# Performance work log

Measured on AMD Instinct MI355X. Metric: run time of the kernel, lower is better.

The kernel has to match this reference:

```python
import jax, jax.numpy as jnp
import numpy as np

L, B, H, IN = 4, 256, 1024, 1024

def setup_inputs() -> dict:
    key = jax.random.key(0)
    ks = jax.random.split(key, 7)
    return {
        "x": jax.random.normal(ks[0], (B, IN), jnp.float32),
        "h0": jax.random.normal(ks[1], (L, B, H), jnp.float32),
        "c0": jax.random.normal(ks[2], (L, B, H), jnp.float32),
        "w_ih": jax.random.normal(ks[3], (L, 4 * H, IN), jnp.float32) * 0.02,
        "w_hh": jax.random.normal(ks[4], (L, 4 * H, H), jnp.float32) * 0.02,
        "b_ih": jax.random.normal(ks[5], (L, 4 * H), jnp.float32) * 0.02,
        "b_hh": jax.random.normal(ks[6], (L, 4 * H), jnp.float32) * 0.02,
    }

def _lstm_cell(inp, h, c, wi, wh, bi, bh):
    # gates: (B, 4H), PyTorch gate order i, f, g, o
    gates = jnp.dot(inp, wi.T) + jnp.dot(h, wh.T) + bi + bh
    i_g, f_g, g_g, o_g = jnp.split(gates, 4, axis=-1)
    c_new = jax.nn.sigmoid(f_g) * c + jax.nn.sigmoid(i_g) * jnp.tanh(g_g)
    h_new = jax.nn.sigmoid(o_g) * jnp.tanh(c_new)
    return h_new, c_new

def reference(x, h0, c0, w_ih, w_hh, b_ih, b_hh):
    # Sequential over layers (inter-layer dependency); dropout is identity (eval mode / p=0).
    inp = x
    hs, cs = [], []
    for i in range(h0.shape[0]):
        h, c = _lstm_cell(inp, h0[i], c0[i], w_ih[i], w_hh[i], b_ih[i], b_hh[i])
        hs.append(h)
        cs.append(c)
        inp = h
    return jnp.stack(hs, axis=0), jnp.stack(cs, axis=0)
```

## Files before the change

### kernel.cpp

```cpp
#include <hip/hip_runtime.h>

#define NLAYER 4
#define BATCH  256
#define HID    1024

typedef float f32x4 __attribute__((ext_vector_type(4)));
typedef short short8 __attribute__((ext_vector_type(8)));
typedef unsigned short ushort_t;
typedef unsigned long long u64;

#define BAR()     asm volatile("s_barrier")
#define WAITV(n)  asm volatile("s_waitcnt vmcnt(" #n ")")
#define WAITV_TIE2(n, x, y) \
  asm volatile("s_waitcnt vmcnt(" #n ")" : "+v"(x), "+v"(y))
#define DSR(d, a) asm volatile("ds_read_b128 %0, %1" : "=v"(d) : "v"(a))
#define LGKM0_TIE4(a,b,c,d) \
  asm volatile("s_waitcnt lgkmcnt(0)" : "+v"(a),"+v"(b),"+v"(c),"+v"(d))
#define FULLBAR() asm volatile("s_waitcnt vmcnt(0) lgkmcnt(0)\ns_barrier" ::: "memory")
#define GLD16(d, a) asm volatile("global_load_dwordx4 %0, %1, off" : "=v"(d) : "v"(a))
#define WAITV0_TIE8(a,b,c,d,e,f,g,h) \
  asm volatile("s_waitcnt vmcnt(0)" \
               : "+v"(a),"+v"(b),"+v"(c),"+v"(d), \
                 "+v"(e),"+v"(f),"+v"(g),"+v"(h))

__device__ __forceinline__ unsigned short f2bf(float f) {
  unsigned int u = __float_as_uint(f);
  unsigned int r = u + 0x7fffu + ((u >> 16) & 1u);
  return (unsigned short)(r >> 16);
}
__device__ __forceinline__ float sigm(float x) { return 1.f / (1.f + __expf(-x)); }
__device__ __forceinline__ float tanh_(float x) { return 2.f / (1.f + __expf(-2.f * x)) - 1.f; }

__device__ __forceinline__ void dma16(const void* g, void* l) {
  __builtin_amdgcn_global_load_lds(
      (const __attribute__((address_space(1))) unsigned int*)g,
      (__attribute__((address_space(3))) unsigned int*)l, 16, 0, 0);
}


__global__ __launch_bounds__(256) void pack_init(
    const float* __restrict__ x, const float* __restrict__ h0,
    const float* __restrict__ w_ih, const float* __restrict__ w_hh,
    ushort_t* __restrict__ wpk, ushort_t* __restrict__ apk) {
  int blk = blockIdx.x;
  if (blk >= 640) {
    int u = blk - 640;
    int l = u >> 10;
    int qb = (u & 1023) * 1024 + threadIdx.x;
    const float* wi = w_ih + (size_t)l * 4194304;
    const float* wh = w_hh + (size_t)l * 4194304;
    ushort_t* dst = wpk + (size_t)l * 8388608;
    u64 s0, s1, s2, s3;
    {
      u64* sp[4] = {&s0, &s1, &s2, &s3};
#pragma unroll
      for (int j = 0; j < 4; ++j) {
        int q = qb + j * 256;
        int i = q & 63, g = (q >> 6) & 7, kt = (q >> 9) & 31, nbq = q >> 14;
        int r = g * 8 + (i >> 3);
        int c = (i & 7) ^ (r & 7);
        *sp[j] = (u64)(const char*)(((kt >> 4) ? wh : wi)
            + ((size_t)((r >> 4) * 1024 + nbq * 16 + (r & 15)) << 10)
            + ((kt & 15) * 64 + c * 8));
      }
    }
    f32x4 v0a, v0b, v1a, v1b, v2a, v2b, v3a, v3b;
    GLD16(v0a, s0); GLD16(v0b, s0 + 16);
    GLD16(v1a, s1); GLD16(v1b, s1 + 16);
    GLD16(v2a, s2); GLD16(v2b, s2 + 16);
    GLD16(v3a, s3); GLD16(v3b, s3 + 16);
    WAITV0_TIE8(v0a, v0b, v1a, v1b, v2a, v2b, v3a, v3b);
#define PSTORE(J, VA, VB)                                                   \
    {                                                                       \
      short8 pk;                                                            \
      pk[0] = (short)f2bf(VA[0]); pk[1] = (short)f2bf(VA[1]);               \
      pk[2] = (short)f2bf(VA[2]); pk[3] = (short)f2bf(VA[3]);               \
      pk[4] = (short)f2bf(VB[0]); pk[5] = (short)f2bf(VB[1]);               \
      pk[6] = (short)f2bf(VB[2]); pk[7] = (short)f2bf(VB[3]);               \
      *(short8*)(dst + (size_t)(qb + (J) * 256) * 8) = pk;                  \
    }
    PSTORE(0, v0a, v0b)
    PSTORE(1, v1a, v1b)
    PSTORE(2, v2a, v2b)
    PSTORE(3, v3a, v3b)
#undef PSTORE
    return;
  }
  int t = blk * 256 + threadIdx.x;
  int lane = t & 63;
  int r8 = lane >> 3;
  int c = (lane & 7) ^ r8;
  const float* src;
  ushort_t* dst;
  if (t < 32768) {
    int g = (t >> 6) & 7, kt = (t >> 9) & 15, mb = t >> 13;
    int m = mb * 64 + g * 8 + r8;
    src = x + (size_t)m * 1024 + kt * 64 + c * 8;
    dst = apk + (size_t)mb * 131072 + (size_t)kt * 4096 + g * 512 + lane * 8;
  } else {
    int u = t - 32768;
    int g = (u >> 6) & 7, kt16 = (u >> 9) & 15, mb = (u >> 13) & 3, l = u >> 15;
    int m = mb * 64 + g * 8 + r8;
    src = h0 + (size_t)l * 262144 + (size_t)m * 1024 + kt16 * 64 + c * 8;
    dst = apk + (size_t)l * 524288 + (size_t)mb * 131072
        + (size_t)(16 + kt16) * 4096 + g * 512 + lane * 8;
  }
  float4 a = *(const float4*)src, b = *(const float4*)(src + 4);
  short8 pk;
  pk[0] = (short)f2bf(a.x); pk[1] = (short)f2bf(a.y);
  pk[2] = (short)f2bf(a.z); pk[3] = (short)f2bf(a.w);
  pk[4] = (short)f2bf(b.x); pk[5] = (short)f2bf(b.y);
  pk[6] = (short)f2bf(b.z); pk[7] = (short)f2bf(b.w);
  *(short8*)dst = pk;
}

__global__ __launch_bounds__(512) void lstm_fused(
    const ushort_t* __restrict__ apk, const ushort_t* __restrict__ wpk,
    const float* __restrict__ bi, const float* __restrict__ bh,
    const float* __restrict__ c0l,
    float* __restrict__ hout, float* __restrict__ cout,
    ushort_t* __restrict__ apk_next) {
  __shared__ union U {
    ushort_t stage[4][4096];
    float sg[4 * 64 * 17];
  } sm;

  const int tid = threadIdx.x;
  const int nb = blockIdx.x;
  const int mb = blockIdx.y;
  const int h0c = nb * 16;
  const int m0 = mb * 64;
  const int lane = tid & 63;
  const int w = tid >> 6;
  const int wm = w & 3, wcol = w >> 2;
  const int lrow = lane & 15, lq = lane >> 4;

  const char* srcB = (const char*)(wpk + (size_t)nb * 131072 + w * 512 + lane * 8);

  const int rA = wm * 16 + lrow;
#define CHUNK(r, c) (((r) >> 3) * 64 + ((r) & 7) * 8 + (((c) ^ (r)) & 7))
  u64 aA0 = (u64)(const char*)(apk + (size_t)mb * 131072 + CHUNK(rA, lq) * 8);
  u64 aA1 = (u64)(const char*)(apk + (size_t)mb * 131072 + CHUNK(rA, 4 + lq) * 8);

  unsigned smb = (unsigned)(uintptr_t)(__attribute__((address_space(3))) void*)&sm;
  const int rB0 = wcol * 32 + lrow, rB1 = rB0 + 16;
  unsigned oB00 = smb + CHUNK(rB0, lq) * 16, oB01 = smb + CHUNK(rB0, 4 + lq) * 16;
  unsigned oB10 = smb + CHUNK(rB1, lq) * 16, oB11 = smb + CHUNK(rB1, 4 + lq) * 16;
#undef CHUNK

  f32x4 acc0 = {0.f, 0.f, 0.f, 0.f}, acc1 = {0.f, 0.f, 0.f, 0.f};
  short8 areg[4][2];

#pragma unroll
  for (int t = 0; t < 3; ++t) {
    dma16(srcB, &sm.stage[t][w * 512]);
    srcB += 8192;
    GLD16(areg[t][0], aA0); aA0 += 8192;
    GLD16(areg[t][1], aA1); aA1 += 8192;
  }

#define KSTEP(S, PRE, POST, ISSUE)                                          \
  {                                                                         \
    WAITV(PRE);                                                             \
    BAR();                                                                  \
    if (ISSUE) {                                                            \
      dma16(srcB, &sm.stage[(S + 3) & 3][w * 512]);                         \
      srcB += 8192;                                                         \
      GLD16(areg[(S + 3) & 3][0], aA0); aA0 += 8192;                        \
      GLD16(areg[(S + 3) & 3][1], aA1); aA1 += 8192;                        \
    }                                                                       \
    WAITV_TIE2(POST, areg[S][0], areg[S][1]);                               \
    short8 b00, b01, b10, b11;                                              \
    DSR(b00, oB00 + (S) * 8192u); DSR(b10, oB10 + (S) * 8192u);             \
    DSR(b01, oB01 + (S) * 8192u); DSR(b11, oB11 + (S) * 8192u);             \
    LGKM0_TIE4(b00, b01, b10, b11);                                         \
    acc0 = __builtin_amdgcn_mfma_f32_16x16x32_bf16(areg[S][0], b00, acc0, 0, 0, 0); \
    acc1 = __builtin_amdgcn_mfma_f32_16x16x32_bf16(areg[S][0], b10, acc1, 0, 0, 0); \
    acc0 = __builtin_amdgcn_mfma_f32_16x16x32_bf16(areg[S][1], b01, acc0, 0, 0, 0); \
    acc1 = __builtin_amdgcn_mfma_f32_16x16x32_bf16(areg[S][1], b11, acc1, 0, 0, 0); \
  }

  for (int i = 0; i < 7; ++i) {
    KSTEP(0, 8, 9, 1)
    KSTEP(1, 8, 9, 1)
    KSTEP(2, 8, 9, 1)
    KSTEP(3, 8, 9, 1)
  }
  KSTEP(0, 8, 9, 1)
  KSTEP(1, 8, 6, 0)
  KSTEP(2, 5, 3, 0)
  KSTEP(3, 2, 0, 0)
#undef KSTEP

  FULLBAR();

#pragma unroll
  for (int nt = 0; nt < 2; ++nt) {
    int gate = wcol * 2 + nt;
    int rowb = wm * 16 + lq * 4;
    const f32x4& a = nt ? acc1 : acc0;
#pragma unroll
    for (int r = 0; r < 4; ++r)
      sm.sg[gate * 1088 + (rowb + r) * 17 + lrow] = a[r];
  }
  FULLBAR();

  {
    const int erow = tid >> 3, ehp = (tid & 7) * 2;
    float2 cp = *(const float2*)(c0l + (size_t)(m0 + erow) * 1024 + h0c + ehp);
    float cpa[2] = {cp.x, cp.y};
    float hva[2], cva[2];
#pragma unroll
    for (int e = 0; e < 2; ++e) {
      int hc = ehp + e;
      float gi = sm.sg[0 * 1088 + erow * 17 + hc] + bi[h0c + hc]          + bh[h0c + hc];
      float gf = sm.sg[1 * 1088 + erow * 17 + hc] + bi[1024 + h0c + hc]   + bh[1024 + h0c + hc];
      float gg = sm.sg[2 * 1088 + erow * 17 + hc] + bi[2048 + h0c + hc]   + bh[2048 + h0c + hc];
      float go = sm.sg[3 * 1088 + erow * 17 + hc] + bi[3072 + h0c + hc]   + bh[3072 + h0c + hc];
      float cn = sigm(gf) * cpa[e] + sigm(gi) * tanh_(gg);
      cva[e] = cn;
      hva[e] = sigm(go) * tanh_(cn);
    }
    float2 hv; hv.x = hva[0]; hv.y = hva[1];
    float2 cv; cv.x = cva[0]; cv.y = cva[1];
    *(float2*)(hout + (size_t)(m0 + erow) * 1024 + h0c + ehp) = hv;
    *(float2*)(cout + (size_t)(m0 + erow) * 1024 + h0c + ehp) = cv;
    if (apk_next) {
      int g = erow >> 3;
#pragma unroll
      for (int e = 0; e < 2; ++e) {
        int k = h0c + ehp + e;
        int cc = (k >> 3) & 7, j = k & 7;
        int i = (erow & 7) * 8 + ((cc ^ erow) & 7);
        apk_next[(size_t)mb * 131072 + (size_t)(k >> 6) * 4096 + g * 512 + i * 8 + j] =
            f2bf(hva[e]);
      }
    }
  }
}

extern "C" void kernel_launch(void* const* d_in, const int* in_sizes, int n_in,
                              void* d_out, int out_size, void* d_ws, size_t ws_size,
                              hipStream_t stream) {
  const float* x    = (const float*)d_in[0];
  const float* h0   = (const float*)d_in[1];
  const float* c0   = (const float*)d_in[2];
  const float* w_ih = (const float*)d_in[3];
  const float* w_hh = (const float*)d_in[4];
  const float* b_ih = (const float*)d_in[5];
  const float* b_hh = (const float*)d_in[6];
  float* out = (float*)d_out;

  ushort_t* Wpk = (ushort_t*)d_ws;
  ushort_t* Apk = Wpk + (size_t)4 * 8388608;

  pack_init<<<4736, 256, 0, stream>>>(x, h0, w_ih, w_hh, Wpk, Apk);

  const size_t BH = (size_t)BATCH * HID;
  for (int l = 0; l < NLAYER; ++l) {
    lstm_fused<<<dim3(64, 4), 512, 0, stream>>>(
        Apk + (size_t)l * 524288, Wpk + (size_t)l * 8388608,
        b_ih + (size_t)l * 4096, b_hh + (size_t)l * 4096,
        c0 + (size_t)l * BH,
        out + (size_t)l * BH, out + (size_t)NLAYER * BH + (size_t)l * BH,
        (l < NLAYER - 1) ? Apk + (size_t)(l + 1) * 524288 : (ushort_t*)nullptr);
  }
}
```

Before: 222.6 us.

## Halve M-tile to 32 rows, doubling grid to 512 blocks

Each block now covers 32 batch rows instead of 64, so the grid grows from 256 to 512 blocks and more of the MI355X CUs get work. Each wave now computes one 16x16 gate tile instead of two, and the epilogue handles one element per thread. The cost is that the full packed weight slice is streamed through LDS twice as often, doubling weight traffic from L2/HBM, and each wave does half the MFMA work per LDS barrier.

```diff
diff --git a/kernel.cpp b/kernel.cpp
--- a/kernel.cpp
+++ b/kernel.cpp
@@ -14,8 +14,8 @@
 #define WAITV_TIE2(n, x, y) \
   asm volatile("s_waitcnt vmcnt(" #n ")" : "+v"(x), "+v"(y))
 #define DSR(d, a) asm volatile("ds_read_b128 %0, %1" : "=v"(d) : "v"(a))
-#define LGKM0_TIE4(a,b,c,d) \
-  asm volatile("s_waitcnt lgkmcnt(0)" : "+v"(a),"+v"(b),"+v"(c),"+v"(d))
+#define LGKM0_TIE2(a,b) \
+  asm volatile("s_waitcnt lgkmcnt(0)" : "+v"(a),"+v"(b))
 #define FULLBAR() asm volatile("s_waitcnt vmcnt(0) lgkmcnt(0)\ns_barrier" ::: "memory")
 #define GLD16(d, a) asm volatile("global_load_dwordx4 %0, %1, off" : "=v"(d) : "v"(a))
 #define WAITV0_TIE8(a,b,c,d,e,f,g,h) \
@@ -122,33 +122,34 @@
     ushort_t* __restrict__ apk_next) {
   __shared__ union U {
     ushort_t stage[4][4096];
-    float sg[4 * 64 * 17];
+    float sg[4 * 32 * 17];
   } sm;
 
   const int tid = threadIdx.x;
   const int nb = blockIdx.x;
-  const int mb = blockIdx.y;
+  const int mby = blockIdx.y;
+  const int mbp = mby >> 1;
   const int h0c = nb * 16;
-  const int m0 = mb * 64;
+  const int m0 = mby * 32;
   const int lane = tid & 63;
   const int w = tid >> 6;
-  const int wm = w & 3, wcol = w >> 2;
+  const int wm = w & 1;
+  const int wcol = w >> 1;
   const int lrow = lane & 15, lq = lane >> 4;
 
   const char* srcB = (const char*)(wpk + (size_t)nb * 131072 + w * 512 + lane * 8);
 
-  const int rA = wm * 16 + lrow;
+  const int rA = (mby & 1) * 32 + wm * 16 + lrow;
 #define CHUNK(r, c) (((r) >> 3) * 64 + ((r) & 7) * 8 + (((c) ^ (r)) & 7))
-  u64 aA0 = (u64)(const char*)(apk + (size_t)mb * 131072 + CHUNK(rA, lq) * 8);
-  u64 aA1 = (u64)(const char*)(apk + (size_t)mb * 131072 + CHUNK(rA, 4 + lq) * 8);
+  u64 aA0 = (u64)(const char*)(apk + (size_t)mbp * 131072 + CHUNK(rA, lq) * 8);
+  u64 aA1 = (u64)(const char*)(apk + (size_t)mbp * 131072 + CHUNK(rA, 4 + lq) * 8);
 
   unsigned smb = (unsigned)(uintptr_t)(__attribute__((address_space(3))) void*)&sm;
-  const int rB0 = wcol * 32 + lrow, rB1 = rB0 + 16;
+  const int rB0 = wcol * 16 + lrow;
   unsigned oB00 = smb + CHUNK(rB0, lq) * 16, oB01 = smb + CHUNK(rB0, 4 + lq) * 16;
-  unsigned oB10 = smb + CHUNK(rB1, lq) * 16, oB11 = smb + CHUNK(rB1, 4 + lq) * 16;
 #undef CHUNK
 
-  f32x4 acc0 = {0.f, 0.f, 0.f, 0.f}, acc1 = {0.f, 0.f, 0.f, 0.f};
+  f32x4 acc0 = {0.f, 0.f, 0.f, 0.f};
   short8 areg[4][2];
 
 #pragma unroll
@@ -170,14 +171,12 @@
       GLD16(areg[(S + 3) & 3][1], aA1); aA1 += 8192;                        \
     }                                                                       \
     WAITV_TIE2(POST, areg[S][0], areg[S][1]);                               \
-    short8 b00, b01, b10, b11;                                              \
-    DSR(b00, oB00 + (S) * 8192u); DSR(b10, oB10 + (S) * 8192u);             \
-    DSR(b01, oB01 + (S) * 8192u); DSR(b11, oB11 + (S) * 8192u);             \
-    LGKM0_TIE4(b00, b01, b10, b11);                                         \
+    short8 b00, b01;                                                        \
+    DSR(b00, oB00 + (S) * 8192u);                                           \
+    DSR(b01, oB01 + (S) * 8192u);                                           \
+    LGKM0_TIE2(b00, b01);                                                   \
     acc0 = __builtin_amdgcn_mfma_f32_16x16x32_bf16(areg[S][0], b00, acc0, 0, 0, 0); \
-    acc1 = __builtin_amdgcn_mfma_f32_16x16x32_bf16(areg[S][0], b10, acc1, 0, 0, 0); \
     acc0 = __builtin_amdgcn_mfma_f32_16x16x32_bf16(areg[S][1], b01, acc0, 0, 0, 0); \
-    acc1 = __builtin_amdgcn_mfma_f32_16x16x32_bf16(areg[S][1], b11, acc1, 0, 0, 0); \
   }
 
   for (int i = 0; i < 7; ++i) {
@@ -195,46 +194,33 @@
   FULLBAR();
 
 #pragma unroll
-  for (int nt = 0; nt < 2; ++nt) {
-    int gate = wcol * 2 + nt;
-    int rowb = wm * 16 + lq * 4;
-    const f32x4& a = nt ? acc1 : acc0;
-#pragma unroll
-    for (int r = 0; r < 4; ++r)
-      sm.sg[gate * 1088 + (rowb + r) * 17 + lrow] = a[r];
-  }
+  for (int r = 0; r < 4; ++r)
+    sm.sg[wcol * 544 + (wm * 16 + lq * 4 + r) * 17 + lrow] = acc0[r];
   FULLBAR();
 
   {
-    const int erow = tid >> 3, ehp = (tid & 7) * 2;
-    float2 cp = *(const float2*)(c0l + (size_t)(m0 + erow) * 1024 + h0c + ehp);
-    float cpa[2] = {cp.x, cp.y};
-    float hva[2], cva[2];
-#pragma unroll
-    for (int e = 0; e < 2; ++e) {
-      int hc = ehp + e;
-      float gi = sm.sg[0 * 1088 + erow * 17 + hc] + bi[h0c + hc]          + bh[h0c + hc];
-      float gf = sm.sg[1 * 1088 + erow * 17 + hc] + bi[1024 + h0c + hc]   + bh[1024 + h0c + hc];
-      float gg = sm.sg[2 * 1088 + erow * 17 + hc] + bi[2048 + h0c + hc]   + bh[2048 + h0c + hc];
-      float go = sm.sg[3 * 1088 + erow * 17 + hc] + bi[3072 + h0c + hc]   + bh[3072 + h0c + hc];
-      float cn = sigm(gf) * cpa[e] + sigm(gi) * tanh_(gg);
-      cva[e] = cn;
-      hva[e] = sigm(go) * tanh_(cn);
-    }
-    float2 hv; hv.x = hva[0]; hv.y = hva[1];
-    float2 cv; cv.x = cva[0]; cv.y = cva[1];
-    *(float2*)(hout + (size_t)(m0 + erow) * 1024 + h0c + ehp) = hv;
-    *(float2*)(cout + (size_t)(m0 + erow) * 1024 + h0c + ehp) = cv;
+    const int erow = tid >> 4;
+    const int eh = tid & 15;
+    const int hc = h0c + eh;
+    const size_t grow = (size_t)(m0 + erow) * 1024 + hc;
+    float cp = c0l[grow];
+    float gi = sm.sg[0 * 544 + erow * 17 + eh] + bi[hc]        + bh[hc];
+    float gf = sm.sg[1 * 544 + erow * 17 + eh] + bi[1024 + hc] + bh[1024 + hc];
+    float gg = sm.sg[2 * 544 + erow * 17 + eh] + bi[2048 + hc] + bh[2048 + hc];
+    float go = sm.sg[3 * 544 + erow * 17 + eh] + bi[3072 + hc] + bh[3072 + hc];
+    float cn = sigm(gf) * cp + sigm(gi) * tanh_(gg);
+    float hv = sigm(go) * tanh_(cn);
+    hout[grow] = hv;
+    cout[grow] = cn;
     if (apk_next) {
-      int g = erow >> 3;
-#pragma unroll
-      for (int e = 0; e < 2; ++e) {
-        int k = h0c + ehp + e;
-        int cc = (k >> 3) & 7, j = k & 7;
-        int i = (erow & 7) * 8 + ((cc ^ erow) & 7);
-        apk_next[(size_t)mb * 131072 + (size_t)(k >> 6) * 4096 + g * 512 + i * 8 + j] =
-            f2bf(hva[e]);
-      }
+      int m = m0 + erow;
+      int mrow = m & 63;
+      int k = hc;
+      int cc = (k >> 3) & 7, j = k & 7;
+      int i = (mrow & 7) * 8 + ((cc ^ mrow) & 7);
+      int g = mrow >> 3;
+      apk_next[(size_t)(m >> 6) * 131072 + (size_t)(k >> 6) * 4096
+               + g * 512 + i * 8 + j] = f2bf(hv);
     }
   }
 }
@@ -258,7 +244,7 @@
 
   const size_t BH = (size_t)BATCH * HID;
   for (int l = 0; l < NLAYER; ++l) {
-    lstm_fused<<<dim3(64, 4), 512, 0, stream>>>(
+    lstm_fused<<<dim3(64, 8), 512, 0, stream>>>(
         Apk + (size_t)l * 524288, Wpk + (size_t)l * 8388608,
         b_ih + (size_t)l * 4096, b_hh + (size_t)l * 4096,
         c0 + (size_t)l * BH,
```

Result: slower. 244.5 us (+9.8%).

## Load weight tiles directly into registers instead of staging through LDS

Applied to the files above, without the earlier changes.

The pack kernel now writes weights in a per-lane MFMA fragment order, so the LSTM GEMM kernel can load B operands straight from global memory into registers with dwordx4 loads. This removes the LDS staging buffer, the per-k-step block barrier and the ds_read round trip, and uses vmcnt waits that cover both A and B loads. The cost is that weight tiles shared by four M-waves are no longer shared through LDS, so each wave fetches its B fragments itself, which raises global/L2 traffic and register use.

```diff
diff --git a/kernel.cpp b/kernel.cpp
--- a/kernel.cpp
+++ b/kernel.cpp
@@ -9,15 +9,11 @@
 typedef unsigned short ushort_t;
 typedef unsigned long long u64;
 
-#define BAR()     asm volatile("s_barrier")
-#define WAITV(n)  asm volatile("s_waitcnt vmcnt(" #n ")")
-#define WAITV_TIE2(n, x, y) \
-  asm volatile("s_waitcnt vmcnt(" #n ")" : "+v"(x), "+v"(y))
-#define DSR(d, a) asm volatile("ds_read_b128 %0, %1" : "=v"(d) : "v"(a))
-#define LGKM0_TIE4(a,b,c,d) \
-  asm volatile("s_waitcnt lgkmcnt(0)" : "+v"(a),"+v"(b),"+v"(c),"+v"(d))
 #define FULLBAR() asm volatile("s_waitcnt vmcnt(0) lgkmcnt(0)\ns_barrier" ::: "memory")
 #define GLD16(d, a) asm volatile("global_load_dwordx4 %0, %1, off" : "=v"(d) : "v"(a))
+#define WAITV_TIE6(n, a,b,c,d,e,f) \
+  asm volatile("s_waitcnt vmcnt(" #n ")" \
+               : "+v"(a),"+v"(b),"+v"(c),"+v"(d),"+v"(e),"+v"(f))
 #define WAITV0_TIE8(a,b,c,d,e,f,g,h) \
   asm volatile("s_waitcnt vmcnt(0)" \
                : "+v"(a),"+v"(b),"+v"(c),"+v"(d), \
@@ -30,12 +26,6 @@
 }
 __device__ __forceinline__ float sigm(float x) { return 1.f / (1.f + __expf(-x)); }
 __device__ __forceinline__ float tanh_(float x) { return 2.f / (1.f + __expf(-2.f * x)) - 1.f; }
-
-__device__ __forceinline__ void dma16(const void* g, void* l) {
-  __builtin_amdgcn_global_load_lds(
-      (const __attribute__((address_space(1))) unsigned int*)g,
-      (__attribute__((address_space(3))) unsigned int*)l, 16, 0, 0);
-}
 
 
 __global__ __launch_bounds__(256) void pack_init(
@@ -72,12 +62,19 @@
     WAITV0_TIE8(v0a, v0b, v1a, v1b, v2a, v2b, v3a, v3b);
 #define PSTORE(J, VA, VB)                                                   \
     {                                                                       \
+      int q = qb + (J) * 256;                                               \
+      int i = q & 63, g = (q >> 6) & 7;                                     \
+      int r = g * 8 + (i >> 3);                                             \
+      int c = (i & 7) ^ (r & 7);                                            \
+      int dd = ((r >> 5) << 8) | (((r >> 4) & 1) << 7) | ((c >> 2) << 6)    \
+             | ((c & 3) << 4) | (r & 15);                                   \
+      size_t nq = (((size_t)(q >> 9)) << 9) | (size_t)dd;                   \
       short8 pk;                                                            \
       pk[0] = (short)f2bf(VA[0]); pk[1] = (short)f2bf(VA[1]);               \
       pk[2] = (short)f2bf(VA[2]); pk[3] = (short)f2bf(VA[3]);               \
       pk[4] = (short)f2bf(VB[0]); pk[5] = (short)f2bf(VB[1]);               \
       pk[6] = (short)f2bf(VB[2]); pk[7] = (short)f2bf(VB[3]);               \
-      *(short8*)(dst + (size_t)(qb + (J) * 256) * 8) = pk;                  \
+      *(short8*)(dst + nq * 8) = pk;                                        \
     }
     PSTORE(0, v0a, v0b)
     PSTORE(1, v1a, v1b)
@@ -120,10 +117,7 @@
     const float* __restrict__ c0l,
     float* __restrict__ hout, float* __restrict__ cout,
     ushort_t* __restrict__ apk_next) {
-  __shared__ union U {
-    ushort_t stage[4][4096];
-    float sg[4 * 64 * 17];
-  } sm;
+  __shared__ float sg[4 * 64 * 17];
 
   const int tid = threadIdx.x;
   const int nb = blockIdx.x;
@@ -135,61 +129,61 @@
   const int wm = w & 3, wcol = w >> 2;
   const int lrow = lane & 15, lq = lane >> 4;
 
-  const char* srcB = (const char*)(wpk + (size_t)nb * 131072 + w * 512 + lane * 8);
+  const char* wbase = (const char*)wpk + (size_t)nb * 262144
+                    + wcol * 4096 + lane * 16;
+  u64 bB0 = (u64)wbase;
+  u64 bB1 = (u64)wbase + 1024;
+  u64 bB2 = (u64)wbase + 2048;
+  u64 bB3 = (u64)wbase + 3072;
 
   const int rA = wm * 16 + lrow;
 #define CHUNK(r, c) (((r) >> 3) * 64 + ((r) & 7) * 8 + (((c) ^ (r)) & 7))
   u64 aA0 = (u64)(const char*)(apk + (size_t)mb * 131072 + CHUNK(rA, lq) * 8);
   u64 aA1 = (u64)(const char*)(apk + (size_t)mb * 131072 + CHUNK(rA, 4 + lq) * 8);
-
-  unsigned smb = (unsigned)(uintptr_t)(__attribute__((address_space(3))) void*)&sm;
-  const int rB0 = wcol * 32 + lrow, rB1 = rB0 + 16;
-  unsigned oB00 = smb + CHUNK(rB0, lq) * 16, oB01 = smb + CHUNK(rB0, 4 + lq) * 16;
-  unsigned oB10 = smb + CHUNK(rB1, lq) * 16, oB11 = smb + CHUNK(rB1, 4 + lq) * 16;
 #undef CHUNK
 
   f32x4 acc0 = {0.f, 0.f, 0.f, 0.f}, acc1 = {0.f, 0.f, 0.f, 0.f};
+  short8 breg[4][4];
   short8 areg[4][2];
 
 #pragma unroll
   for (int t = 0; t < 3; ++t) {
-    dma16(srcB, &sm.stage[t][w * 512]);
-    srcB += 8192;
+    GLD16(breg[t][0], bB0); bB0 += 8192;
+    GLD16(breg[t][1], bB1); bB1 += 8192;
+    GLD16(breg[t][2], bB2); bB2 += 8192;
+    GLD16(breg[t][3], bB3); bB3 += 8192;
     GLD16(areg[t][0], aA0); aA0 += 8192;
     GLD16(areg[t][1], aA1); aA1 += 8192;
   }
 
-#define KSTEP(S, PRE, POST, ISSUE)                                          \
+#define KSTEP(S, N, ISSUE)                                                  \
   {                                                                         \
-    WAITV(PRE);                                                             \
-    BAR();                                                                  \
     if (ISSUE) {                                                            \
-      dma16(srcB, &sm.stage[(S + 3) & 3][w * 512]);                         \
-      srcB += 8192;                                                         \
+      GLD16(breg[(S + 3) & 3][0], bB0); bB0 += 8192;                        \
+      GLD16(breg[(S + 3) & 3][1], bB1); bB1 += 8192;                        \
+      GLD16(breg[(S + 3) & 3][2], bB2); bB2 += 8192;                        \
+      GLD16(breg[(S + 3) & 3][3], bB3); bB3 += 8192;                        \
       GLD16(areg[(S + 3) & 3][0], aA0); aA0 += 8192;                        \
       GLD16(areg[(S + 3) & 3][1], aA1); aA1 += 8192;                        \
     }                                                                       \
-    WAITV_TIE2(POST, areg[S][0], areg[S][1]);                               \
-    short8 b00, b01, b10, b11;                                              \
-    DSR(b00, oB00 + (S) * 8192u); DSR(b10, oB10 + (S) * 8192u);             \
-    DSR(b01, oB01 + (S) * 8192u); DSR(b11, oB11 + (S) * 8192u);             \
-    LGKM0_TIE4(b00, b01, b10, b11);                                         \
-    acc0 = __builtin_amdgcn_mfma_f32_16x16x32_bf16(areg[S][0], b00, acc0, 0, 0, 0); \
-    acc1 = __builtin_amdgcn_mfma_f32_16x16x32_bf16(areg[S][0], b10, acc1, 0, 0, 0); \
-    acc0 = __builtin_amdgcn_mfma_f32_16x16x32_bf16(areg[S][1], b01, acc0, 0, 0, 0); \
-    acc1 = __builtin_amdgcn_mfma_f32_16x16x32_bf16(areg[S][1], b11, acc1, 0, 0, 0); \
+    WAITV_TIE6(N, breg[S][0], breg[S][1], breg[S][2], breg[S][3],           \
+               areg[S][0], areg[S][1]);                                     \
+    acc0 = __builtin_amdgcn_mfma_f32_16x16x32_bf16(areg[S][0], breg[S][0], acc0, 0, 0, 0); \
+    acc1 = __builtin_amdgcn_mfma_f32_16x16x32_bf16(areg[S][0], breg[S][2], acc1, 0, 0, 0); \
+    acc0 = __builtin_amdgcn_mfma_f32_16x16x32_bf16(areg[S][1], breg[S][1], acc0, 0, 0, 0); \
+    acc1 = __builtin_amdgcn_mfma_f32_16x16x32_bf16(areg[S][1], breg[S][3], acc1, 0, 0, 0); \
   }
 
   for (int i = 0; i < 7; ++i) {
-    KSTEP(0, 8, 9, 1)
-    KSTEP(1, 8, 9, 1)
-    KSTEP(2, 8, 9, 1)
-    KSTEP(3, 8, 9, 1)
-  }
-  KSTEP(0, 8, 9, 1)
-  KSTEP(1, 8, 6, 0)
-  KSTEP(2, 5, 3, 0)
-  KSTEP(3, 2, 0, 0)
+    KSTEP(0, 18, 1)
+    KSTEP(1, 18, 1)
+    KSTEP(2, 18, 1)
+    KSTEP(3, 18, 1)
+  }
+  KSTEP(0, 18, 1)
+  KSTEP(1, 12, 0)
+  KSTEP(2, 6, 0)
+  KSTEP(3, 0, 0)
 #undef KSTEP
 
   FULLBAR();
@@ -201,7 +195,7 @@
     const f32x4& a = nt ? acc1 : acc0;
 #pragma unroll
     for (int r = 0; r < 4; ++r)
-      sm.sg[gate * 1088 + (rowb + r) * 17 + lrow] = a[r];
+      sg[gate * 1088 + (rowb + r) * 17 + lrow] = a[r];
   }
   FULLBAR();
 
@@ -213,10 +207,10 @@
 #pragma unroll
     for (int e = 0; e < 2; ++e) {
       int hc = ehp + e;
-      float gi = sm.sg[0 * 1088 + erow * 17 + hc] + bi[h0c + hc]          + bh[h0c + hc];
-      float gf = sm.sg[1 * 1088 + erow * 17 + hc] + bi[1024 + h0c + hc]   + bh[1024 + h0c + hc];
-      float gg = sm.sg[2 * 1088 + erow * 17 + hc] + bi[2048 + h0c + hc]   + bh[2048 + h0c + hc];
-      float go = sm.sg[3 * 1088 + erow * 17 + hc] + bi[3072 + h0c + hc]   + bh[3072 + h0c + hc];
+      float gi = sg[0 * 1088 + erow * 17 + hc] + bi[h0c + hc]          + bh[h0c + hc];
+      float gf = sg[1 * 1088 + erow * 17 + hc] + bi[1024 + h0c + hc]   + bh[1024 + h0c + hc];
+      float gg = sg[2 * 1088 + erow * 17 + hc] + bi[2048 + h0c + hc]   + bh[2048 + h0c + hc];
+      float go = sg[3 * 1088 + erow * 17 + hc] + bi[3072 + h0c + hc]   + bh[3072 + h0c + hc];
       float cn = sigm(gf) * cpa[e] + sigm(gi) * tanh_(gg);
       cva[e] = cn;
       hva[e] = sigm(go) * tanh_(cn);
```

Result: slower. 240.1 us (+7.9%).

## Stage A operand through LDS via async DMA and split weight packing per layer

Applied to the files above, without the earlier changes.

The activation (A) tiles in the fused LSTM GEMM are now loaded with global-to-LDS DMA into a second 4-stage LDS ring, the same way the weights already were, instead of global loads straight into registers. The vmcnt waits are retuned to match, and the MFMA operands now all come from ds_read. Separately, the single large pack kernel is split into one launch per layer, with the activation packing attached only to the first. This frees A registers and unifies the pipeline, but doubles LDS staging and adds extra launches.

```diff
diff --git a/kernel.cpp b/kernel.cpp
--- a/kernel.cpp
+++ b/kernel.cpp
@@ -11,11 +11,10 @@
 
 #define BAR()     asm volatile("s_barrier")
 #define WAITV(n)  asm volatile("s_waitcnt vmcnt(" #n ")")
-#define WAITV_TIE2(n, x, y) \
-  asm volatile("s_waitcnt vmcnt(" #n ")" : "+v"(x), "+v"(y))
 #define DSR(d, a) asm volatile("ds_read_b128 %0, %1" : "=v"(d) : "v"(a))
-#define LGKM0_TIE4(a,b,c,d) \
-  asm volatile("s_waitcnt lgkmcnt(0)" : "+v"(a),"+v"(b),"+v"(c),"+v"(d))
+#define LGKM0_TIE6(a,b,c,d,e,f) \
+  asm volatile("s_waitcnt lgkmcnt(0)" \
+               : "+v"(a),"+v"(b),"+v"(c),"+v"(d),"+v"(e),"+v"(f))
 #define FULLBAR() asm volatile("s_waitcnt vmcnt(0) lgkmcnt(0)\ns_barrier" ::: "memory")
 #define GLD16(d, a) asm volatile("global_load_dwordx4 %0, %1, off" : "=v"(d) : "v"(a))
 #define WAITV0_TIE8(a,b,c,d,e,f,g,h) \
@@ -40,16 +39,12 @@
 
 __global__ __launch_bounds__(256) void pack_init(
     const float* __restrict__ x, const float* __restrict__ h0,
-    const float* __restrict__ w_ih, const float* __restrict__ w_hh,
-    ushort_t* __restrict__ wpk, ushort_t* __restrict__ apk) {
+    const float* __restrict__ wi, const float* __restrict__ wh,
+    ushort_t* __restrict__ wdst, ushort_t* __restrict__ apk, int awork) {
   int blk = blockIdx.x;
-  if (blk >= 640) {
-    int u = blk - 640;
-    int l = u >> 10;
-    int qb = (u & 1023) * 1024 + threadIdx.x;
-    const float* wi = w_ih + (size_t)l * 4194304;
-    const float* wh = w_hh + (size_t)l * 4194304;
-    ushort_t* dst = wpk + (size_t)l * 8388608;
+  if (blk >= awork) {
+    int u = blk - awork;
+    int qb = u * 1024 + threadIdx.x;
     u64 s0, s1, s2, s3;
     {
       u64* sp[4] = {&s0, &s1, &s2, &s3};
@@ -77,7 +72,7 @@
       pk[2] = (short)f2bf(VA[2]); pk[3] = (short)f2bf(VA[3]);               \
       pk[4] = (short)f2bf(VB[0]); pk[5] = (short)f2bf(VB[1]);               \
       pk[6] = (short)f2bf(VB[2]); pk[7] = (short)f2bf(VB[3]);               \
-      *(short8*)(dst + (size_t)(qb + (J) * 256) * 8) = pk;                  \
+      *(short8*)(wdst + (size_t)(qb + (J) * 256) * 8) = pk;                 \
     }
     PSTORE(0, v0a, v0b)
     PSTORE(1, v1a, v1b)
@@ -121,7 +116,7 @@
     float* __restrict__ hout, float* __restrict__ cout,
     ushort_t* __restrict__ apk_next) {
   __shared__ union U {
-    ushort_t stage[4][4096];
+    struct { ushort_t A[4][4096]; ushort_t B[4][4096]; } st;
     float sg[4 * 64 * 17];
   } sm;
 
@@ -135,61 +130,59 @@
   const int wm = w & 3, wcol = w >> 2;
   const int lrow = lane & 15, lq = lane >> 4;
 
-  const char* srcB = (const char*)(wpk + (size_t)nb * 131072 + w * 512 + lane * 8);
-
+  const char* srcB = (const char*)(wpk + (size_t)nb * 131072) + w * 1024 + lane * 16;
+  const char* srcA = (const char*)(apk + (size_t)mb * 131072) + w * 1024 + lane * 16;
+
+#define CHUNK(r, c) (((r) >> 3) * 64 + ((r) & 7) * 8 + (((c) ^ (r)) & 7))
+  unsigned smb = (unsigned)(uintptr_t)(__attribute__((address_space(3))) void*)&sm;
   const int rA = wm * 16 + lrow;
-#define CHUNK(r, c) (((r) >> 3) * 64 + ((r) & 7) * 8 + (((c) ^ (r)) & 7))
-  u64 aA0 = (u64)(const char*)(apk + (size_t)mb * 131072 + CHUNK(rA, lq) * 8);
-  u64 aA1 = (u64)(const char*)(apk + (size_t)mb * 131072 + CHUNK(rA, 4 + lq) * 8);
-
-  unsigned smb = (unsigned)(uintptr_t)(__attribute__((address_space(3))) void*)&sm;
+  unsigned oA0 = smb + CHUNK(rA, lq) * 16;
+  unsigned oA1 = smb + CHUNK(rA, 4 + lq) * 16;
   const int rB0 = wcol * 32 + lrow, rB1 = rB0 + 16;
-  unsigned oB00 = smb + CHUNK(rB0, lq) * 16, oB01 = smb + CHUNK(rB0, 4 + lq) * 16;
-  unsigned oB10 = smb + CHUNK(rB1, lq) * 16, oB11 = smb + CHUNK(rB1, 4 + lq) * 16;
+  unsigned oB00 = smb + 32768u + CHUNK(rB0, lq) * 16;
+  unsigned oB01 = smb + 32768u + CHUNK(rB0, 4 + lq) * 16;
+  unsigned oB10 = smb + 32768u + CHUNK(rB1, lq) * 16;
+  unsigned oB11 = smb + 32768u + CHUNK(rB1, 4 + lq) * 16;
 #undef CHUNK
 
   f32x4 acc0 = {0.f, 0.f, 0.f, 0.f}, acc1 = {0.f, 0.f, 0.f, 0.f};
-  short8 areg[4][2];
 
 #pragma unroll
   for (int t = 0; t < 3; ++t) {
-    dma16(srcB, &sm.stage[t][w * 512]);
-    srcB += 8192;
-    GLD16(areg[t][0], aA0); aA0 += 8192;
-    GLD16(areg[t][1], aA1); aA1 += 8192;
-  }
-
-#define KSTEP(S, PRE, POST, ISSUE)                                          \
+    dma16(srcB, &sm.st.B[t][w * 512]); srcB += 8192;
+    dma16(srcA, &sm.st.A[t][w * 512]); srcA += 8192;
+  }
+
+#define KSTEP(S, PRE, ISSUE)                                                \
   {                                                                         \
     WAITV(PRE);                                                             \
     BAR();                                                                  \
     if (ISSUE) {                                                            \
-      dma16(srcB, &sm.stage[(S + 3) & 3][w * 512]);                         \
-      srcB += 8192;                                                         \
-      GLD16(areg[(S + 3) & 3][0], aA0); aA0 += 8192;                        \
-      GLD16(areg[(S + 3) & 3][1], aA1); aA1 += 8192;                        \
+      const int S3 = ((S) + 3) & 3;                                         \
+      dma16(srcB, &sm.st.B[S3][w * 512]); srcB += 8192;                     \
+      dma16(srcA, &sm.st.A[S3][w * 512]); srcA += 8192;                     \
     }                                                                       \
-    WAITV_TIE2(POST, areg[S][0], areg[S][1]);                               \
-    short8 b00, b01, b10, b11;                                              \
+    short8 a0, a1, b00, b01, b10, b11;                                      \
+    DSR(a0, oA0 + (S) * 8192u); DSR(a1, oA1 + (S) * 8192u);                 \
     DSR(b00, oB00 + (S) * 8192u); DSR(b10, oB10 + (S) * 8192u);             \
     DSR(b01, oB01 + (S) * 8192u); DSR(b11, oB11 + (S) * 8192u);             \
-    LGKM0_TIE4(b00, b01, b10, b11);                                         \
-    acc0 = __builtin_amdgcn_mfma_f32_16x16x32_bf16(areg[S][0], b00, acc0, 0, 0, 0); \
-    acc1 = __builtin_amdgcn_mfma_f32_16x16x32_bf16(areg[S][0], b10, acc1, 0, 0, 0); \
-    acc0 = __builtin_amdgcn_mfma_f32_16x16x32_bf16(areg[S][1], b01, acc0, 0, 0, 0); \
-    acc1 = __builtin_amdgcn_mfma_f32_16x16x32_bf16(areg[S][1], b11, acc1, 0, 0, 0); \
+    LGKM0_TIE6(a0, a1, b00, b01, b10, b11);                                 \
+    acc0 = __builtin_amdgcn_mfma_f32_16x16x32_bf16(a0, b00, acc0, 0, 0, 0); \
+    acc1 = __builtin_amdgcn_mfma_f32_16x16x32_bf16(a0, b10, acc1, 0, 0, 0); \
+    acc0 = __builtin_amdgcn_mfma_f32_16x16x32_bf16(a1, b01, acc0, 0, 0, 0); \
+    acc1 = __builtin_amdgcn_mfma_f32_16x16x32_bf16(a1, b11, acc1, 0, 0, 0); \
   }
 
   for (int i = 0; i < 7; ++i) {
-    KSTEP(0, 8, 9, 1)
-    KSTEP(1, 8, 9, 1)
-    KSTEP(2, 8, 9, 1)
-    KSTEP(3, 8, 9, 1)
-  }
-  KSTEP(0, 8, 9, 1)
-  KSTEP(1, 8, 6, 0)
-  KSTEP(2, 5, 3, 0)
-  KSTEP(3, 2, 0, 0)
+    KSTEP(0, 4, 1)
+    KSTEP(1, 4, 1)
+    KSTEP(2, 4, 1)
+    KSTEP(3, 4, 1)
+  }
+  KSTEP(0, 4, 1)
+  KSTEP(1, 4, 0)
+  KSTEP(2, 2, 0)
+  KSTEP(3, 0, 0)
 #undef KSTEP
 
   FULLBAR();
@@ -254,7 +247,12 @@
   ushort_t* Wpk = (ushort_t*)d_ws;
   ushort_t* Apk = Wpk + (size_t)4 * 8388608;
 
-  pack_init<<<4736, 256, 0, stream>>>(x, h0, w_ih, w_hh, Wpk, Apk);
+  for (int l = 0; l < NLAYER; ++l) {
+    int awork = (l == 0) ? 640 : 0;
+    pack_init<<<1024 + awork, 256, 0, stream>>>(
+        x, h0, w_ih + (size_t)l * 4194304, w_hh + (size_t)l * 4194304,
+        Wpk + (size_t)l * 8388608, Apk, awork);
+  }
 
   const size_t BH = (size_t)BATCH * HID;
   for (int l = 0; l < NLAYER; ++l) {
```

Measured after the change: 227.2 us. +2.0%, slower.
